# Kernel optimization log

Measured on AMD Instinct MI355X. Metric: run time of the kernel, lower is better.

## Reference

```python
import jax, jax.numpy as jnp
import numpy as np

B, V, L = 128, 128000, 200


def setup_inputs() -> dict:
    key = jax.random.key(0)
    k1, k2, k3, k4, k5, k6, k7 = jax.random.split(key, 7)
    return {
        "logits": jax.random.normal(k1, (B, V), dtype=jnp.float32),
        "presence_penalties": jax.random.uniform(k2, (B,), dtype=jnp.float32, minval=0.0, maxval=2.0),
        "frequency_penalties": jax.random.uniform(k3, (B,), dtype=jnp.float32, minval=0.0, maxval=2.0),
        "temperatures": jax.random.uniform(k4, (B,), dtype=jnp.float32, minval=0.5, maxval=1.5),
        "top_ps": jax.random.uniform(k5, (B,), dtype=jnp.float32, minval=0.7, maxval=1.0),
        "output_tokens": jax.random.randint(k6, (B, L), 0, V),
        "top_ks": jax.random.randint(k7, (B,), 1, 1000),
    }


def reference(logits, presence_penalties, frequency_penalties, temperatures,
              top_ps, output_tokens, top_ks):
    b, v = logits.shape
    # --- penalties: batched bincount via scatter-add (matches _batched_bincount,
    # including counting the 0-padded history tokens, as the torch code does) ---
    rows = jnp.arange(b)[:, None]
    occ = jnp.zeros((b, v), dtype=logits.dtype).at[rows, output_tokens].add(1.0)
    logits = logits - occ * frequency_penalties[:, None] \
                    - (occ > 0).astype(logits.dtype) * presence_penalties[:, None]
    # --- temperature ---
    logits = logits / temperatures[:, None]
    # --- top-p / top-k filtering (sort descending, mask, unsort) ---
    idx = jnp.argsort(-logits, axis=-1)                       # [b, v] descending order
    logits_sort = jnp.take_along_axis(logits, idx, axis=-1)
    probs_sort = jax.nn.softmax(logits_sort, axis=-1)
    probs_cum = jnp.cumsum(probs_sort, axis=-1)
    top_p_mask = (probs_cum - probs_sort) > top_ps[:, None]
    top_k_mask = jnp.arange(v)[None, :] >= top_ks[:, None]
    logits_sort = jnp.where(top_p_mask | top_k_mask, -jnp.inf, logits_sort)
    inv = jnp.argsort(idx, axis=-1)
    logits = jnp.take_along_axis(logits_sort, inv, axis=-1)   # back to vocab order
    # --- probs / logprobs ---
    probs = jax.nn.softmax(logits, axis=-1)
    logprobs = jax.nn.log_softmax(logits, axis=-1)
    # --- multinomial sample via Gumbel-max (deterministic fixed key) ---
    g = jax.random.gumbel(jax.random.key(42), (b, v), dtype=logits.dtype)
    next_tokens = jnp.argmax(logprobs + g, axis=-1)
    return probs, logprobs, next_tokens
```

## Files before the change

kernel.cpp:

```cpp
#include <hip/hip_runtime.h>
#include <stdint.h>


#define B_ 128
#define V_ 128000
#define V4_ (V_ / 4)
#define L_ 200
#define NBIN_ 8192
#define RCAP_ 4608
#define TCAP_ 2048

#define JAX_PARTITIONABLE 1

__device__ __forceinline__ uint32_t f2key(float f) {
  uint32_t u = __float_as_uint(f);
  return (u & 0x80000000u) ? ~u : (u | 0x80000000u);
}
__device__ __forceinline__ float key2f(uint32_t k) {
  uint32_t u = (k & 0x80000000u) ? (k ^ 0x80000000u) : ~k;
  return __uint_as_float(u);
}
__device__ __forceinline__ float binhi(uint32_t bin) {
  return key2f((bin << 19) | 0x7FFFFu);
}

__device__ __forceinline__ float adj_pen(float x, float cnt, float fp, float pp, float tt) {
#pragma clang fp contract(off)
  return ((x - cnt * fp) - pp) / tt;
}
__device__ __forceinline__ float adj_plain(float x, float tt) {
#pragma clang fp contract(off)
  return x / tt;
}
__device__ __forceinline__ float fsub(float a, float b) {
#pragma clang fp contract(off)
  return a - b;
}

__device__ __forceinline__ void tf_round(uint32_t &a, uint32_t &b, int r) {
  a += b;
  b = (b << r) | (b >> (32 - r));
  b ^= a;
}
__device__ __forceinline__ void threefry2x32(uint32_t x0, uint32_t x1, uint32_t &o0, uint32_t &o1) {
  const uint32_t k0 = 0u, k1 = 42u;
  const uint32_t k2 = k0 ^ k1 ^ 0x1BD11BDAu;
  x0 += k0; x1 += k1;
  tf_round(x0, x1, 13); tf_round(x0, x1, 15); tf_round(x0, x1, 26); tf_round(x0, x1, 6);
  x0 += k1; x1 += k2 + 1u;
  tf_round(x0, x1, 17); tf_round(x0, x1, 29); tf_round(x0, x1, 16); tf_round(x0, x1, 24);
  x0 += k2; x1 += k0 + 2u;
  tf_round(x0, x1, 13); tf_round(x0, x1, 15); tf_round(x0, x1, 26); tf_round(x0, x1, 6);
  x0 += k0; x1 += k1 + 3u;
  tf_round(x0, x1, 17); tf_round(x0, x1, 29); tf_round(x0, x1, 16); tf_round(x0, x1, 24);
  x0 += k1; x1 += k2 + 4u;
  tf_round(x0, x1, 13); tf_round(x0, x1, 15); tf_round(x0, x1, 26); tf_round(x0, x1, 6);
  x0 += k2; x1 += k0 + 5u;
  o0 = x0; o1 = x1;
}
__device__ __forceinline__ float gumbel_at(uint32_t j) {
  uint32_t o0, o1, bits;
#if JAX_PARTITIONABLE
  threefry2x32(0u, j, o0, o1);
  bits = o0 ^ o1;
#else
  const uint32_t half = (uint32_t)B_ * (uint32_t)V_ / 2u;
  if (j < half) { threefry2x32(j, j + half, o0, o1); bits = o0; }
  else          { threefry2x32(j - half, j, o0, o1); bits = o1; }
#endif
  float u = __uint_as_float((bits >> 9) | 0x3f800000u) - 1.0f;
  float r = (u == 0.0f) ? 1.17549435e-38f : u;
  return -logf(-logf(r));
}

__global__ void __launch_bounds__(1024) k_fused_v12(
    const float* __restrict__ logits, const float* __restrict__ pres,
    const float* __restrict__ freq, const float* __restrict__ temps,
    const float* __restrict__ topps, const int* __restrict__ toks,
    const int* __restrict__ topks,
    float* __restrict__ probs, float* __restrict__ Ylp, float* __restrict__ tail) {
  const int b = blockIdx.x, tid = threadIdx.x;
  __shared__ uint32_t lhist[NBIN_];
  __shared__ uint32_t lk[RCAP_];
  __shared__ uint32_t li[RCAP_];
  __shared__ uint32_t bmap[V_ / 32];
  __shared__ int stok[L_];
  __shared__ uint32_t ptok[L_];
  __shared__ uint32_t pyv[L_];
  __shared__ uint32_t tlist[TCAP_];
  __shared__ uint32_t ccnt[256];
  __shared__ float cw[256];
  __shared__ float zcw[256];
  __shared__ uint32_t mb[256];
  __shared__ uint32_t lh[256];
  __shared__ float rf[1024];
  __shared__ unsigned long long ru[1024];
  __shared__ uint32_t s_lcnt, s_pcnt, s_r, s_prefix, s_pmask, s_tieE, s_tiemax, s_tcnt;
  __shared__ float s_m;

  if (tid < L_) stok[tid] = toks[b * L_ + tid];
  for (int i = tid; i < NBIN_; i += 1024) lhist[i] = 0u;
  for (int i = tid; i < V_ / 32; i += 1024) bmap[i] = 0u;
  if (tid == 0) { s_lcnt = 0u; s_pcnt = 0u; s_tiemax = 0x7FFFFFFFu; s_tcnt = 0u; }
  const float tt = temps[b];
  const uint32_t kth = f2key(adj_plain(2.0f, tt));
  __syncthreads();

  const float4* src = (const float4*)(logits + (size_t)b * V_);
  for (int it = 0; it < 32; ++it) {
    const int i4 = it * 1024 + tid;
    if (i4 < V4_) {
      const float4 x = src[i4];
      const float vv[4] = {adj_plain(x.x, tt), adj_plain(x.y, tt),
                           adj_plain(x.z, tt), adj_plain(x.w, tt)};
      const int v0 = i4 * 4;
#pragma unroll
      for (int p = 0; p < 4; ++p) {
        const uint32_t k = f2key(vv[p]);
        atomicAdd(&lhist[k >> 19], 1u);
        if (k >= kth) {
          const uint32_t slot = atomicAdd(&s_lcnt, 1u);
          if (slot < RCAP_) { lk[slot] = k; li[slot] = (uint32_t)(v0 + p); }
        }
      }
    }
  }
  __syncthreads();

  if (tid < L_) {
    const int t0 = stok[tid];
    int cnt = 0; bool first = true;
    for (int i = 0; i < L_; ++i) {
      const int ti = stok[i];
      cnt += (ti == t0);
      if (i < tid && ti == t0) first = false;
    }
    if (first) {
      const float x = logits[(size_t)b * V_ + t0];
      const float y_old = adj_plain(x, tt);
      const float y_new = adj_pen(x, (float)cnt, freq[b], pres[b], tt);
      atomicSub(&lhist[f2key(y_old) >> 19], 1u);
      atomicAdd(&lhist[f2key(y_new) >> 19], 1u);
      atomicOr(&bmap[t0 >> 5], 1u << (t0 & 31));
      const uint32_t slot = atomicAdd(&s_pcnt, 1u);
      if (slot < (uint32_t)L_) {
        ptok[slot] = (uint32_t)t0;
        pyv[slot] = __float_as_uint(y_new);
      }
    }
  }
  __syncthreads();

  const uint32_t C = s_lcnt < RCAP_ ? s_lcnt : RCAP_;
  for (uint32_t i = tid; i < C; i += 1024) {
    const uint32_t idx = li[i];
    if (bmap[idx >> 5] & (1u << (idx & 31))) {
      int cnt = 0;
      for (int j = 0; j < L_; ++j) cnt += (stok[j] == (int)idx);
      const float x = logits[(size_t)b * V_ + idx];
      lk[i] = f2key(adj_pen(x, (float)cnt, freq[b], pres[b], tt));
    }
  }
  __syncthreads();

  if (tid < 256) {
    uint32_t sc = 0; float sw = 0.0f; uint32_t mymb = 0u;
    const int hi = (NBIN_ - 1) - 32 * tid;
    for (int i = 0; i < 32; ++i) {
      const int bin = hi - i;
      const uint32_t c = lhist[bin];
      sc += c;
      if (c) {
        sw += (float)c * __expf(binhi((uint32_t)bin));
        if ((uint32_t)bin > mymb) mymb = (uint32_t)bin;
      }
    }
    ccnt[tid] = sc; cw[tid] = sw; zcw[tid] = sw; mb[tid] = mymb;
  }
  __syncthreads();
  for (int s = 128; s > 0; s >>= 1) {
    if (tid < s) {
      mb[tid] = mb[tid] > mb[tid + s] ? mb[tid] : mb[tid + s];
      zcw[tid] += zcw[tid + s];
    }
    __syncthreads();
  }

  if (tid == 0) {
    s_m = binhi(mb[0]);
    const float Z = zcw[0];
    const float limit = topps[b] * Z;
    const uint32_t K = (uint32_t)topks[b];
    uint32_t np = (uint32_t)V_;
    {
      float cm = 0.0f; uint32_t cc = 0; bool done = false;
      for (int k = 0; k < 256 && !done; ++k) {
        if (cm + cw[k] > limit) {
          const int hh = (NBIN_ - 1) - 32 * k;
          for (int i = 0; i < 32; ++i) {
            const int bin = hh - i;
            const uint32_t c = lhist[bin];
            float rm = 0.0f;
            if (c) rm = (float)c * __expf(binhi((uint32_t)bin));
            cc += c; cm += rm;
            if (cm > limit) { np = cc; done = true; break; }
          }
        } else { cm += cw[k]; cc += ccnt[k]; }
      }
    }
    uint32_t n = K < np ? K : np;
    if (n < 1u) n = 1u;
    uint32_t istar = 0, cab = 0;
    {
      uint32_t cc = 0;
      for (int k = 0; k < 256; ++k) {
        if (cc + ccnt[k] >= n) {
          const int hh = (NBIN_ - 1) - 32 * k;
          for (int i = 0; i < 32; ++i) {
            const int bin = hh - i;
            if (cc + lhist[bin] >= n) { istar = (uint32_t)bin; cab = cc; break; }
            cc += lhist[bin];
          }
          break;
        } else cc += ccnt[k];
      }
    }
    s_r = n - cab;
    s_prefix = istar << 19;
    s_pmask = 0xFFF80000u;
  }
  __syncthreads();
  const float m = s_m;

  const int shifts[3] = {11, 3, 0};
  const uint32_t widths[3] = {256u, 256u, 8u};
  for (int p = 0; p < 3; ++p) {
    const int sh = shifts[p];
    const uint32_t w = widths[p];
    for (uint32_t i = tid; i < w; i += 1024) lh[i] = 0u;
    __syncthreads();
    const uint32_t pr = s_prefix, pm = s_pmask;
    for (uint32_t c = tid; c < C; c += 1024) {
      const uint32_t k = lk[c];
      if ((k & pm) == pr) atomicAdd(&lh[(k >> sh) & (w - 1u)], 1u);
    }
    __syncthreads();
    if (tid == 0) {
      const uint32_t rr = s_r;
      uint32_t cum = 0; int found = -1;
      for (int bkt = (int)w - 1; bkt >= 0; --bkt) {
        if (cum + lh[bkt] >= rr) { found = bkt; break; }
        cum += lh[bkt];
      }
      if (found < 0) { found = 0; cum = rr > 0 ? rr - 1u : 0u; }
      s_r = rr - cum;
      s_prefix = pr | ((uint32_t)found << sh);
      s_pmask = pm | ((w - 1u) << sh);
      s_tieE = lh[found];
    }
    __syncthreads();
  }
  const uint32_t tkey = s_prefix;
  const uint32_t ekeep = s_r;
  const uint32_t E = s_tieE;
  __syncthreads();

  if (ekeep < E && E <= (uint32_t)TCAP_) {
    for (uint32_t c = tid; c < C; c += 1024) {
      if (lk[c] == tkey) {
        const uint32_t pos = atomicAdd(&s_tcnt, 1u);
        if (pos < (uint32_t)TCAP_) tlist[pos] = li[c];
      }
    }
    __syncthreads();
    const uint32_t tc = s_tcnt < (uint32_t)TCAP_ ? s_tcnt : (uint32_t)TCAP_;
    for (uint32_t i = tid; i < tc; i += 1024) {
      const uint32_t mine = tlist[i];
      uint32_t rank = 0;
      for (uint32_t j = 0; j < tc; ++j) rank += (tlist[j] < mine) ? 1u : 0u;
      if (rank == ekeep - 1u) s_tiemax = mine;
    }
    __syncthreads();
  }
  const uint32_t tiemax = s_tiemax;

  float zp = 0.0f;
  for (uint32_t c = tid; c < C; c += 1024) {
    const uint32_t k = lk[c];
    if (k > tkey || (k == tkey && li[c] <= tiemax)) zp += expf(fsub(key2f(k), m));
  }
  rf[tid] = zp;
  __syncthreads();
  for (int s = 512; s > 0; s >>= 1) { if (tid < s) rf[tid] += rf[tid + s]; __syncthreads(); }
  const float Zp = rf[0];
  const float logZp = logf(Zp);

  unsigned long long best = 0ull;
  for (uint32_t c = tid; c < C; c += 1024) {
    const uint32_t k = lk[c];
    const uint32_t idx = li[c];
    if (k > tkey || (k == tkey && idx <= tiemax)) {
      const float lp = fsub(fsub(key2f(k), m), logZp);
      const float g = gumbel_at((uint32_t)b * (uint32_t)V_ + idx);
      const float sv = lp + g;
      const unsigned long long pk =
          ((unsigned long long)f2key(sv) << 32) | (unsigned long long)(~idx);
      if (pk > best) best = pk;
    }
  }
  ru[tid] = best;
  __syncthreads();
  for (int s = 512; s > 0; s >>= 1) {
    if (tid < s) ru[tid] = ru[tid] > ru[tid + s] ? ru[tid] : ru[tid + s];
    __syncthreads();
  }
  if (tid == 0) {
    const uint32_t bi = ~((uint32_t)(ru[0] & 0xFFFFFFFFull));
    tail[b] = (float)bi;
  }
  __syncthreads();

  const float nbig = -1e38f;
  float4* pdst = (float4*)(probs + (size_t)b * V_);
  float4* ldst = (float4*)(Ylp + (size_t)b * V_);
  for (int it = 0; it < 32; ++it) {
    const int i4 = it * 1024 + tid;
    if (i4 < V4_) {
      const float4 x = src[i4];
      const int v0 = i4 * 4;
      const float xx[4] = {x.x, x.y, x.z, x.w};
      float py[4], ly[4];
#pragma unroll
      for (int p = 0; p < 4; ++p) {
        const float yy = adj_plain(xx[p], tt);
        const uint32_t ky = f2key(yy);
        const bool kept = (ky > tkey) || (ky == tkey && (uint32_t)(v0 + p) <= tiemax);
        const float d = fsub(yy, m);
        py[p] = kept ? (expf(d) / Zp) : 0.0f;
        ly[p] = kept ? fsub(d, logZp) : nbig;
      }
      float4 p4; p4.x = py[0]; p4.y = py[1]; p4.z = py[2]; p4.w = py[3];
      float4 l4; l4.x = ly[0]; l4.y = ly[1]; l4.z = ly[2]; l4.w = ly[3];
      pdst[i4] = p4;
      ldst[i4] = l4;
    }
  }
  __syncthreads();

  const uint32_t pcnt = s_pcnt < (uint32_t)L_ ? s_pcnt : (uint32_t)L_;
  for (uint32_t i = tid; i < pcnt; i += 1024) {
    const uint32_t idx = ptok[i];
    const float y = __uint_as_float(pyv[i]);
    const uint32_t ky = f2key(y);
    const bool kept = (ky > tkey) || (ky == tkey && idx <= tiemax);
    const float d = fsub(y, m);
    probs[(size_t)b * V_ + idx] = kept ? (expf(d) / Zp) : 0.0f;
    Ylp[(size_t)b * V_ + idx] = kept ? fsub(d, logZp) : nbig;
  }
}

extern "C" void kernel_launch(void* const* d_in, const int* in_sizes, int n_in,
                              void* d_out, int out_size, void* d_ws, size_t ws_size,
                              hipStream_t stream) {
  (void)in_sizes; (void)n_in; (void)out_size; (void)d_ws; (void)ws_size;
  const float* logits = (const float*)d_in[0];
  const float* pres   = (const float*)d_in[1];
  const float* freq   = (const float*)d_in[2];
  const float* temps  = (const float*)d_in[3];
  const float* topps  = (const float*)d_in[4];
  const int*   toks   = (const int*)d_in[5];
  const int*   topks  = (const int*)d_in[6];
  float* probs = (float*)d_out;
  float* Ylp   = probs + (size_t)B_ * V_;
  float* tail  = probs + 2 * (size_t)B_ * V_;

  k_fused_v12<<<dim3(B_), dim3(1024), 0, stream>>>(
      logits, pres, freq, temps, topps, toks, topks, probs, Ylp, tail);
}
```

Baseline: 288.6 us.

## Split each row across two cooperative blocks with grid sync relay

Each batch row is now handled by two blocks, each scanning half the vocabulary. The second half's histogram and candidate list are passed through the probs output buffer as scratch, with grid.sync between phases. The point is to use 256 blocks instead of 128 on a GPU with more CUs than rows. The serial top-p and radix-select scans are also turned into parallel prefix scans. The cost is two grid-wide barriers and global relay traffic, with a fallback to the old kernel if the cooperative launch fails.

```diff
diff --git a/kernel.cpp b/kernel.cpp
--- a/kernel.cpp
+++ b/kernel.cpp
@@ -1,14 +1,27 @@
 #include <hip/hip_runtime.h>
+#include <hip/hip_cooperative_groups.h>
 #include <stdint.h>
+
+namespace cg = cooperative_groups;
 
 
 #define B_ 128
 #define V_ 128000
+#define H_ (V_ / 2)
+#define H4_ (H_ / 4)
 #define V4_ (V_ / 4)
 #define L_ 200
 #define NBIN_ 8192
-#define RCAP_ 4608
+#define PCAPH_ 2304
+#define RCAP_ (2 * PCAPH_)
 #define TCAP_ 2048
+
+#define REL_STAT_ 0
+#define REL_CCNT_ 8
+#define REL_CAND_ 16
+#define REL_HIST_ 8192
+static_assert(REL_CAND_ + 2 * PCAPH_ <= REL_HIST_, "relay layout");
+static_assert(REL_HIST_ + NBIN_ <= H_, "relay layout");
 
 #define JAX_PARTITIONABLE 1
 
@@ -73,7 +86,397 @@
   return -logf(-logf(r));
 }
 
-__global__ void __launch_bounds__(1024) k_fused_v12(
+__global__ void __launch_bounds__(1024) k_fused_v13(
+    const float* __restrict__ logits, const float* __restrict__ pres,
+    const float* __restrict__ freq, const float* __restrict__ temps,
+    const float* __restrict__ topps, const int* __restrict__ toks,
+    const int* __restrict__ topks,
+    float* __restrict__ probs, float* __restrict__ Ylp, float* __restrict__ tail) {
+  cg::grid_group grid = cg::this_grid();
+  const int b = blockIdx.x >> 1;
+  const int h = blockIdx.x & 1;
+  const int tid = threadIdx.x;
+
+  __shared__ uint32_t lhist[NBIN_];
+  __shared__ uint32_t lk[RCAP_];
+  __shared__ uint32_t li[RCAP_];
+  __shared__ uint32_t bmap[H_ / 32];
+  __shared__ int stok[L_];
+  __shared__ uint32_t ptok[L_];
+  __shared__ uint32_t pyv[L_];
+  __shared__ uint32_t tlist[TCAP_];
+  __shared__ uint32_t ccnt[256];
+  __shared__ float cw[256];
+  __shared__ float zcw[256];
+  __shared__ uint32_t mb[256];
+  __shared__ uint32_t lh[256];
+  __shared__ float scm[256];
+  __shared__ uint32_t scc[256];
+  __shared__ uint32_t sS[256];
+  __shared__ float rf[1024];
+  __shared__ unsigned long long ru[1024];
+  __shared__ uint32_t sstat[5];
+  __shared__ uint32_t s_lcnt, s_pcnt, s_r, s_prefix, s_pmask, s_tieE, s_tiemax, s_tcnt, s_C, s_n;
+  __shared__ int s_pick, s_pick2, s_found;
+  __shared__ float s_m;
+
+  uint32_t* base2u = (uint32_t*)(probs + (size_t)b * V_ + H_);
+
+  if (tid < L_) stok[tid] = toks[b * L_ + tid];
+  for (int i = tid; i < NBIN_; i += 1024) lhist[i] = 0u;
+  for (int i = tid; i < H_ / 32; i += 1024) bmap[i] = 0u;
+  if (tid == 0) { s_lcnt = 0u; s_pcnt = 0u; s_tiemax = 0x7FFFFFFFu; s_tcnt = 0u; }
+  const float tt = temps[b];
+  const uint32_t kth = f2key(adj_plain(2.0f, tt));
+  __syncthreads();
+
+  const int lo = h * H_;
+  const float4* src = (const float4*)(logits + (size_t)b * V_);
+  for (int it = 0; it < 16; ++it) {
+    const int i4 = it * 1024 + tid;
+    if (i4 < H4_) {
+      const int g4 = h * H4_ + i4;
+      const float4 x = src[g4];
+      const float vv[4] = {adj_plain(x.x, tt), adj_plain(x.y, tt),
+                           adj_plain(x.z, tt), adj_plain(x.w, tt)};
+      const int v0 = g4 * 4;
+#pragma unroll
+      for (int p = 0; p < 4; ++p) {
+        const uint32_t k = f2key(vv[p]);
+        atomicAdd(&lhist[k >> 19], 1u);
+        if (k >= kth) {
+          const uint32_t slot = atomicAdd(&s_lcnt, 1u);
+          if (slot < PCAPH_) { lk[slot] = k; li[slot] = (uint32_t)(v0 + p); }
+        }
+      }
+    }
+  }
+  __syncthreads();
+
+  if (tid < L_) {
+    const int t0 = stok[tid];
+    if (t0 >= lo && t0 < lo + H_) {
+      int cnt = 0; bool first = true;
+      for (int i = 0; i < L_; ++i) {
+        const int ti = stok[i];
+        cnt += (ti == t0);
+        if (i < tid && ti == t0) first = false;
+      }
+      if (first) {
+        const float x = logits[(size_t)b * V_ + t0];
+        const float y_old = adj_plain(x, tt);
+        const float y_new = adj_pen(x, (float)cnt, freq[b], pres[b], tt);
+        atomicSub(&lhist[f2key(y_old) >> 19], 1u);
+        atomicAdd(&lhist[f2key(y_new) >> 19], 1u);
+        const int off = t0 - lo;
+        atomicOr(&bmap[off >> 5], 1u << (off & 31));
+        const uint32_t slot = atomicAdd(&s_pcnt, 1u);
+        if (slot < (uint32_t)L_) {
+          ptok[slot] = (uint32_t)t0;
+          pyv[slot] = __float_as_uint(y_new);
+        }
+      }
+    }
+  }
+  __syncthreads();
+
+  const uint32_t myc = s_lcnt < PCAPH_ ? s_lcnt : PCAPH_;
+  for (uint32_t i = tid; i < myc; i += 1024) {
+    const uint32_t idx = li[i];
+    const int off = (int)idx - lo;
+    if (bmap[off >> 5] & (1u << (off & 31))) {
+      int cnt = 0;
+      for (int j = 0; j < L_; ++j) cnt += (stok[j] == (int)idx);
+      const float x = logits[(size_t)b * V_ + idx];
+      lk[i] = f2key(adj_pen(x, (float)cnt, freq[b], pres[b], tt));
+    }
+  }
+  __syncthreads();
+
+  if (h == 1) {
+    if (tid == 0) base2u[REL_CCNT_] = myc;
+    for (uint32_t i = tid; i < myc; i += 1024) {
+      base2u[REL_CAND_ + 2 * i] = lk[i];
+      base2u[REL_CAND_ + 2 * i + 1] = li[i];
+    }
+    for (int i = tid; i < NBIN_; i += 1024) base2u[REL_HIST_ + i] = lhist[i];
+  }
+  __threadfence();
+  grid.sync();
+  __threadfence();
+
+  if (h == 0) {
+    const uint32_t c1r = base2u[REL_CCNT_];
+    const uint32_t c1 = c1r < PCAPH_ ? c1r : PCAPH_;
+    const uint32_t c0 = myc;
+    for (uint32_t i = tid; i < c1; i += 1024) {
+      lk[c0 + i] = base2u[REL_CAND_ + 2 * i];
+      li[c0 + i] = base2u[REL_CAND_ + 2 * i + 1];
+    }
+    for (int i = tid; i < NBIN_; i += 1024) lhist[i] += base2u[REL_HIST_ + i];
+    if (tid == 0) s_C = c0 + c1;
+    __syncthreads();
+    const uint32_t C = s_C;
+
+    if (tid < 256) {
+      uint32_t sc = 0; float sw = 0.0f; uint32_t mymb = 0u;
+      const int hi = (NBIN_ - 1) - 32 * tid;
+      for (int i = 0; i < 32; ++i) {
+        const int bin = hi - i;
+        const uint32_t c = lhist[bin];
+        sc += c;
+        if (c) {
+          sw += (float)c * __expf(binhi((uint32_t)bin));
+          if ((uint32_t)bin > mymb) mymb = (uint32_t)bin;
+        }
+      }
+      ccnt[tid] = sc; cw[tid] = sw; zcw[tid] = sw; mb[tid] = mymb;
+    }
+    __syncthreads();
+    for (int s = 128; s > 0; s >>= 1) {
+      if (tid < s) {
+        mb[tid] = mb[tid] > mb[tid + s] ? mb[tid] : mb[tid + s];
+        zcw[tid] += zcw[tid + s];
+      }
+      __syncthreads();
+    }
+    if (tid == 0) s_m = binhi(mb[0]);
+    const float Z = zcw[0];
+    const float limit = topps[b] * Z;
+
+    if (tid < 256) { scm[tid] = cw[tid]; scc[tid] = ccnt[tid]; }
+    __syncthreads();
+    for (int off = 1; off < 256; off <<= 1) {
+      float a = 0.0f; uint32_t u = 0u;
+      const bool act = (tid < 256 && tid >= off);
+      if (act) { a = scm[tid - off]; u = scc[tid - off]; }
+      __syncthreads();
+      if (act) { scm[tid] += a; scc[tid] += u; }
+      __syncthreads();
+    }
+    if (tid == 0) s_pick = 256;
+    __syncthreads();
+    if (tid < 256) {
+      const float ecm = tid ? scm[tid - 1] : 0.0f;
+      if (ecm + cw[tid] > limit) atomicMin(&s_pick, tid);
+    }
+    __syncthreads();
+    if (tid == 0) {
+      uint32_t np = (uint32_t)V_;
+      const int k = s_pick;
+      if (k < 256) {
+        float cm = k ? scm[k - 1] : 0.0f;
+        uint32_t cc = k ? scc[k - 1] : 0u;
+        const int hh = (NBIN_ - 1) - 32 * k;
+        for (int i = 0; i < 32; ++i) {
+          const int bin = hh - i;
+          const uint32_t c = lhist[bin];
+          float rm = 0.0f;
+          if (c) rm = (float)c * __expf(binhi((uint32_t)bin));
+          cc += c; cm += rm;
+          if (cm > limit) { np = cc; break; }
+        }
+      }
+      const uint32_t K = (uint32_t)topks[b];
+      uint32_t n = K < np ? K : np;
+      if (n < 1u) n = 1u;
+      s_n = n;
+    }
+    __syncthreads();
+    const uint32_t n = s_n;
+    if (tid == 0) s_pick2 = 256;
+    __syncthreads();
+    if (tid < 256) {
+      if (scc[tid] >= n) atomicMin(&s_pick2, tid);
+    }
+    __syncthreads();
+    if (tid == 0) {
+      const int k2 = s_pick2 < 256 ? s_pick2 : 255;
+      uint32_t cc = k2 ? scc[k2 - 1] : 0u;
+      uint32_t istar = 0, cab = 0;
+      const int hh = (NBIN_ - 1) - 32 * k2;
+      for (int i = 0; i < 32; ++i) {
+        const int bin = hh - i;
+        if (cc + lhist[bin] >= n) { istar = (uint32_t)bin; cab = cc; break; }
+        cc += lhist[bin];
+      }
+      s_r = n - cab;
+      s_prefix = istar << 19;
+      s_pmask = 0xFFF80000u;
+    }
+    __syncthreads();
+
+    const int shifts[3] = {11, 3, 0};
+    const uint32_t widths[3] = {256u, 256u, 8u};
+    for (int p = 0; p < 3; ++p) {
+      const int sh = shifts[p];
+      const uint32_t w = widths[p];
+      for (uint32_t i = tid; i < w; i += 1024) lh[i] = 0u;
+      __syncthreads();
+      const uint32_t pr = s_prefix, pm = s_pmask;
+      for (uint32_t c = tid; c < C; c += 1024) {
+        const uint32_t k = lk[c];
+        if ((k & pm) == pr) atomicAdd(&lh[(k >> sh) & (w - 1u)], 1u);
+      }
+      __syncthreads();
+      if (tid < (int)w) sS[tid] = lh[tid];
+      __syncthreads();
+      for (uint32_t off = 1; off < w; off <<= 1) {
+        uint32_t a = 0u;
+        const bool act = (tid + off < w);
+        if (act) a = sS[tid + off];
+        __syncthreads();
+        if (act) sS[tid] += a;
+        __syncthreads();
+      }
+      if (tid == 0) s_found = -1;
+      __syncthreads();
+      const uint32_t rr = s_r;
+      if (tid < (int)w) {
+        const uint32_t Shere = sS[tid];
+        const uint32_t Snext = (tid + 1 < (int)w) ? sS[tid + 1] : 0u;
+        if (Shere >= rr && Snext < rr) s_found = tid;
+      }
+      __syncthreads();
+      if (tid == 0) {
+        int found = s_found;
+        if (found < 0) { found = 0; s_r = 1u; }
+        else {
+          const uint32_t Snext = (found + 1 < (int)w) ? sS[found + 1] : 0u;
+          s_r = rr - Snext;
+        }
+        s_prefix = s_prefix | ((uint32_t)found << sh);
+        s_pmask = s_pmask | ((w - 1u) << sh);
+        s_tieE = lh[found];
+      }
+      __syncthreads();
+    }
+    const uint32_t tkey = s_prefix;
+    const uint32_t ekeep = s_r;
+    const uint32_t E = s_tieE;
+    __syncthreads();
+
+    if (ekeep < E && E <= (uint32_t)TCAP_) {
+      for (uint32_t c = tid; c < C; c += 1024) {
+        if (lk[c] == tkey) {
+          const uint32_t pos = atomicAdd(&s_tcnt, 1u);
+          if (pos < (uint32_t)TCAP_) tlist[pos] = li[c];
+        }
+      }
+      __syncthreads();
+      const uint32_t tc = s_tcnt < (uint32_t)TCAP_ ? s_tcnt : (uint32_t)TCAP_;
+      for (uint32_t i = tid; i < tc; i += 1024) {
+        const uint32_t mine = tlist[i];
+        uint32_t rank = 0;
+        for (uint32_t j = 0; j < tc; ++j) rank += (tlist[j] < mine) ? 1u : 0u;
+        if (rank == ekeep - 1u) s_tiemax = mine;
+      }
+      __syncthreads();
+    }
+    const uint32_t tiemax = s_tiemax;
+    const float m = s_m;
+
+    float zp = 0.0f;
+    for (uint32_t c = tid; c < C; c += 1024) {
+      const uint32_t k = lk[c];
+      if (k > tkey || (k == tkey && li[c] <= tiemax)) zp += expf(fsub(key2f(k), m));
+    }
+    rf[tid] = zp;
+    __syncthreads();
+    for (int s = 512; s > 0; s >>= 1) { if (tid < s) rf[tid] += rf[tid + s]; __syncthreads(); }
+    const float Zp = rf[0];
+    const float logZp = logf(Zp);
+
+    unsigned long long best = 0ull;
+    for (uint32_t c = tid; c < C; c += 1024) {
+      const uint32_t k = lk[c];
+      const uint32_t idx = li[c];
+      if (k > tkey || (k == tkey && idx <= tiemax)) {
+        const float lp = fsub(fsub(key2f(k), m), logZp);
+        const float g = gumbel_at((uint32_t)b * (uint32_t)V_ + idx);
+        const float sv = lp + g;
+        const unsigned long long pk =
+            ((unsigned long long)f2key(sv) << 32) | (unsigned long long)(~idx);
+        if (pk > best) best = pk;
+      }
+    }
+    ru[tid] = best;
+    __syncthreads();
+    for (int s = 512; s > 0; s >>= 1) {
+      if (tid < s) ru[tid] = ru[tid] > ru[tid + s] ? ru[tid] : ru[tid + s];
+      __syncthreads();
+    }
+    if (tid == 0) {
+      tail[b] = (float)(~((uint32_t)(ru[0] & 0xFFFFFFFFull)));
+      base2u[REL_STAT_ + 0] = __float_as_uint(m);
+      base2u[REL_STAT_ + 1] = tkey;
+      base2u[REL_STAT_ + 2] = tiemax;
+      base2u[REL_STAT_ + 3] = __float_as_uint(Zp);
+      base2u[REL_STAT_ + 4] = __float_as_uint(logZp);
+    }
+    __syncthreads();
+  }
+  __threadfence();
+  grid.sync();
+  __threadfence();
+
+  float m_c, Zp_c, logZp_c;
+  uint32_t tkey_c, tiemax_c;
+  if (h == 1) {
+    if (tid < 5) sstat[tid] = base2u[REL_STAT_ + tid];
+    __syncthreads();
+    m_c = __uint_as_float(sstat[0]);
+    tkey_c = sstat[1];
+    tiemax_c = sstat[2];
+    Zp_c = __uint_as_float(sstat[3]);
+    logZp_c = __uint_as_float(sstat[4]);
+  } else {
+    m_c = s_m; tkey_c = s_prefix; tiemax_c = s_tiemax;
+    Zp_c = rf[0]; logZp_c = logf(rf[0]);
+  }
+
+  const float nbig = -1e38f;
+  float4* pdst = (float4*)(probs + (size_t)b * V_);
+  float4* ldst = (float4*)(Ylp + (size_t)b * V_);
+  for (int it = 0; it < 16; ++it) {
+    const int i4 = it * 1024 + tid;
+    if (i4 < H4_) {
+      const int g4 = h * H4_ + i4;
+      const float4 x = src[g4];
+      const int v0 = g4 * 4;
+      const float xx[4] = {x.x, x.y, x.z, x.w};
+      float py[4], ly[4];
+#pragma unroll
+      for (int p = 0; p < 4; ++p) {
+        const float yy = adj_plain(xx[p], tt);
+        const uint32_t ky = f2key(yy);
+        const bool kept = (ky > tkey_c) || (ky == tkey_c && (uint32_t)(v0 + p) <= tiemax_c);
+        const float d = fsub(yy, m_c);
+        py[p] = kept ? (expf(d) / Zp_c) : 0.0f;
+        ly[p] = kept ? fsub(d, logZp_c) : nbig;
+      }
+      float4 p4; p4.x = py[0]; p4.y = py[1]; p4.z = py[2]; p4.w = py[3];
+      float4 l4; l4.x = ly[0]; l4.y = ly[1]; l4.z = ly[2]; l4.w = ly[3];
+      pdst[g4] = p4;
+      ldst[g4] = l4;
+    }
+  }
+  __syncthreads();
+
+  const uint32_t pcnt = s_pcnt < (uint32_t)L_ ? s_pcnt : (uint32_t)L_;
+  for (uint32_t i = tid; i < pcnt; i += 1024) {
+    const uint32_t idx = ptok[i];
+    const float y = __uint_as_float(pyv[i]);
+    const uint32_t ky = f2key(y);
+    const bool kept = (ky > tkey_c) || (ky == tkey_c && idx <= tiemax_c);
+    const float d = fsub(y, m_c);
+    probs[(size_t)b * V_ + idx] = kept ? (expf(d) / Zp_c) : 0.0f;
+    Ylp[(size_t)b * V_ + idx] = kept ? fsub(d, logZp_c) : nbig;
+  }
+}
+
+#define RCAPF_ 4608
+__global__ void __launch_bounds__(1024) k_fused_v12_fb(
     const float* __restrict__ logits, const float* __restrict__ pres,
     const float* __restrict__ freq, const float* __restrict__ temps,
     const float* __restrict__ topps, const int* __restrict__ toks,
@@ -81,8 +484,8 @@
     float* __restrict__ probs, float* __restrict__ Ylp, float* __restrict__ tail) {
   const int b = blockIdx.x, tid = threadIdx.x;
   __shared__ uint32_t lhist[NBIN_];
-  __shared__ uint32_t lk[RCAP_];
-  __shared__ uint32_t li[RCAP_];
+  __shared__ uint32_t lk[RCAPF_];
+  __shared__ uint32_t li[RCAPF_];
   __shared__ uint32_t bmap[V_ / 32];
   __shared__ int stok[L_];
   __shared__ uint32_t ptok[L_];
@@ -105,7 +508,6 @@
   const float tt = temps[b];
   const uint32_t kth = f2key(adj_plain(2.0f, tt));
   __syncthreads();
-
   const float4* src = (const float4*)(logits + (size_t)b * V_);
   for (int it = 0; it < 32; ++it) {
     const int i4 = it * 1024 + tid;
@@ -120,13 +522,12 @@
         atomicAdd(&lhist[k >> 19], 1u);
         if (k >= kth) {
           const uint32_t slot = atomicAdd(&s_lcnt, 1u);
-          if (slot < RCAP_) { lk[slot] = k; li[slot] = (uint32_t)(v0 + p); }
+          if (slot < RCAPF_) { lk[slot] = k; li[slot] = (uint32_t)(v0 + p); }
         }
       }
     }
   }
   __syncthreads();
-
   if (tid < L_) {
     const int t0 = stok[tid];
     int cnt = 0; bool first = true;
@@ -143,15 +544,11 @@
       atomicAdd(&lhist[f2key(y_new) >> 19], 1u);
       atomicOr(&bmap[t0 >> 5], 1u << (t0 & 31));
       const uint32_t slot = atomicAdd(&s_pcnt, 1u);
-      if (slot < (uint32_t)L_) {
-        ptok[slot] = (uint32_t)t0;
-        pyv[slot] = __float_as_uint(y_new);
-      }
-    }
-  }
-  __syncthreads();
-
-  const uint32_t C = s_lcnt < RCAP_ ? s_lcnt : RCAP_;
+      if (slot < (uint32_t)L_) { ptok[slot] = (uint32_t)t0; pyv[slot] = __float_as_uint(y_new); }
+    }
+  }
+  __syncthreads();
+  const uint32_t C = s_lcnt < RCAPF_ ? s_lcnt : RCAPF_;
   for (uint32_t i = tid; i < C; i += 1024) {
     const uint32_t idx = li[i];
     if (bmap[idx >> 5] & (1u << (idx & 31))) {
@@ -162,7 +559,6 @@
     }
   }
   __syncthreads();
-
   if (tid < 256) {
     uint32_t sc = 0; float sw = 0.0f; uint32_t mymb = 0u;
     const int hi = (NBIN_ - 1) - 32 * tid;
@@ -185,7 +581,6 @@
     }
     __syncthreads();
   }
-
   if (tid == 0) {
     s_m = binhi(mb[0]);
     const float Z = zcw[0];
@@ -231,7 +626,6 @@
   }
   __syncthreads();
   const float m = s_m;
-
   const int shifts[3] = {11, 3, 0};
   const uint32_t widths[3] = {256u, 256u, 8u};
   for (int p = 0; p < 3; ++p) {
@@ -264,7 +658,6 @@
   const uint32_t ekeep = s_r;
   const uint32_t E = s_tieE;
   __syncthreads();
-
   if (ekeep < E && E <= (uint32_t)TCAP_) {
     for (uint32_t c = tid; c < C; c += 1024) {
       if (lk[c] == tkey) {
@@ -283,7 +676,6 @@
     __syncthreads();
   }
   const uint32_t tiemax = s_tiemax;
-
   float zp = 0.0f;
   for (uint32_t c = tid; c < C; c += 1024) {
     const uint32_t k = lk[c];
@@ -294,7 +686,6 @@
   for (int s = 512; s > 0; s >>= 1) { if (tid < s) rf[tid] += rf[tid + s]; __syncthreads(); }
   const float Zp = rf[0];
   const float logZp = logf(Zp);
-
   unsigned long long best = 0ull;
   for (uint32_t c = tid; c < C; c += 1024) {
     const uint32_t k = lk[c];
@@ -314,12 +705,8 @@
     if (tid < s) ru[tid] = ru[tid] > ru[tid + s] ? ru[tid] : ru[tid + s];
     __syncthreads();
   }
-  if (tid == 0) {
-    const uint32_t bi = ~((uint32_t)(ru[0] & 0xFFFFFFFFull));
-    tail[b] = (float)bi;
-  }
-  __syncthreads();
-
+  if (tid == 0) tail[b] = (float)(~((uint32_t)(ru[0] & 0xFFFFFFFFull)));
+  __syncthreads();
   const float nbig = -1e38f;
   float4* pdst = (float4*)(probs + (size_t)b * V_);
   float4* ldst = (float4*)(Ylp + (size_t)b * V_);
@@ -346,7 +733,6 @@
     }
   }
   __syncthreads();
-
   const uint32_t pcnt = s_pcnt < (uint32_t)L_ ? s_pcnt : (uint32_t)L_;
   for (uint32_t i = tid; i < pcnt; i += 1024) {
     const uint32_t idx = ptok[i];
@@ -374,6 +760,14 @@
   float* Ylp   = probs + (size_t)B_ * V_;
   float* tail  = probs + 2 * (size_t)B_ * V_;
 
-  k_fused_v12<<<dim3(B_), dim3(1024), 0, stream>>>(
-      logits, pres, freq, temps, topps, toks, topks, probs, Ylp, tail);
-}
+  void* kargs[] = {(void*)&logits, (void*)&pres, (void*)&freq, (void*)&temps,
+                   (void*)&topps, (void*)&toks, (void*)&topks,
+                   (void*)&probs, (void*)&Ylp, (void*)&tail};
+  hipError_t e = hipLaunchCooperativeKernel((void*)k_fused_v13, dim3(2 * B_), dim3(1024),
+                                            kargs, 0, stream);
+  if (e != hipSuccess) {
+    (void)hipGetLastError();
+    k_fused_v12_fb<<<dim3(B_), dim3(1024), 0, stream>>>(
+        logits, pres, freq, temps, topps, toks, topks, probs, Ylp, tail);
+  }
+}
```

New measurement: 548.2 us. 1.9x slower.
